# Kernel tuning notes

Hardware: AMD Instinct MI355X
Metric: run time of the kernel (lower is better)

The kernel has to match this reference:

```python
import jax, jax.numpy as jnp
import numpy as np

NUM_HEADS = 16
SIZE_PER_HEAD = 64
HIDDEN = NUM_HEADS * SIZE_PER_HEAD  # 1024
B, F, T = 4, 1024, 1024
NEG_INF = -10000.0


def setup_inputs() -> dict:
    key = jax.random.key(0)
    ks = jax.random.split(key, 6)
    scale = 0.02
    return {
        "from_tensor": jax.random.normal(ks[0], (B, F, HIDDEN), dtype=jnp.float32),
        "to_tensor": jax.random.normal(ks[1], (B, T, HIDDEN), dtype=jnp.float32),
        "attention_mask": jnp.ones((B, F, T), dtype=jnp.float32),
        "Wq": jax.random.normal(ks[2], (HIDDEN, HIDDEN), dtype=jnp.float32) * scale,
        "bq": jnp.zeros((HIDDEN,), dtype=jnp.float32),
        "Wk": jax.random.normal(ks[3], (HIDDEN, HIDDEN), dtype=jnp.float32) * scale,
        "bk": jnp.zeros((HIDDEN,), dtype=jnp.float32),
        "Wv": jax.random.normal(ks[4], (HIDDEN, HIDDEN), dtype=jnp.float32) * scale,
        "bv": jnp.zeros((HIDDEN,), dtype=jnp.float32),
    }


def _split_heads(x, seq_len):
    # [B, S, H*Dh] -> [B, H, S, Dh]
    return x.reshape(B, seq_len, NUM_HEADS, SIZE_PER_HEAD).transpose(0, 2, 1, 3)


def reference(from_tensor, to_tensor, attention_mask, Wq, bq, Wk, bk, Wv, bv):
    # Q/K/V dense projections (query_act/key_act/value_act are None -> linear)
    q = _split_heads(from_tensor @ Wq + bq, F)   # [B,H,F,Dh]
    k = _split_heads(to_tensor @ Wk + bk, T)     # [B,H,T,Dh]
    v = _split_heads(to_tensor @ Wv + bv, T)     # [B,H,T,Dh]

    # scaled dot-product attention scores: [B,H,F,T]
    scores = jnp.einsum("bhfd,bhtd->bhft", q, k) / jnp.sqrt(
        jnp.asarray(SIZE_PER_HEAD, dtype=q.dtype))

    # BERT-style mask adder: mask==1 -> attend, mask==0 -> -10000
    adder = (1.0 - attention_mask[:, None, :, :]) * NEG_INF
    scores = scores + adder

    attention_probs = jax.nn.softmax(scores, axis=-1)  # dropout_prob=0.0

    ctx = jnp.einsum("bhft,bhtd->bhfd", attention_probs, v)  # [B,H,F,Dh]
    ctx = ctx.transpose(0, 2, 1, 3).reshape(B, F, NUM_HEADS * SIZE_PER_HEAD)
    return ctx, attention_probs
```

## Files before the change

### kernel.cpp

```cpp
#include <hip/hip_runtime.h>

typedef unsigned short u16;
typedef __bf16 bf16x8 __attribute__((ext_vector_type(8)));
typedef float f32x4 __attribute__((ext_vector_type(4)));
typedef u16 u16x8 __attribute__((ext_vector_type(8)));
typedef u16 u16x4 __attribute__((ext_vector_type(4)));

#define NUM_HEADS 16
#define HIDDEN 1024
#define BATCH 4
#define SEQ 1024
#define C1 0.1803368809109783f
#define LOG2E 1.4426950408889634f

#define VMCNT0 asm volatile("s_waitcnt vmcnt(0)" ::: "memory")

static __device__ __forceinline__ u16 f2bf(float x) {
  unsigned u = __float_as_uint(x);
  u = u + 0x7FFFu + ((u >> 16) & 1u);
  return (u16)(u >> 16);
}
static __device__ __forceinline__ float bf2f(u16 b) {
  return __uint_as_float(((unsigned)b) << 16);
}
static __device__ __forceinline__ void async16(u16* lds, const u16* g) {
  __builtin_amdgcn_global_load_lds(
      (const __attribute__((address_space(1))) void*)g,
      (__attribute__((address_space(3))) void*)lds, 16, 0, 0);
}

__global__ void k_cvt(const float* __restrict__ in0, u16* __restrict__ out0,
                      const float* __restrict__ in1, u16* __restrict__ out1, int n8) {
  int i = blockIdx.x * 256 + threadIdx.x;
  if (i >= n8) return;
  const float* in = blockIdx.z ? in1 : in0;
  u16* out = blockIdx.z ? out1 : out0;
  float4 a = ((const float4*)in)[i * 2];
  float4 b = ((const float4*)in)[i * 2 + 1];
  u16x8 v;
  v[0] = f2bf(a.x); v[1] = f2bf(a.y); v[2] = f2bf(a.z); v[3] = f2bf(a.w);
  v[4] = f2bf(b.x); v[5] = f2bf(b.y); v[6] = f2bf(b.z); v[7] = f2bf(b.w);
  *(u16x8*)&out[(size_t)i * 8] = v;
}

__global__ void k_wtrans(const float* __restrict__ Wq, const float* __restrict__ Wk,
                         const float* __restrict__ Wv, u16* __restrict__ Wt) {
  __shared__ float tile[64][65];
  const float* W = (blockIdx.z == 0) ? Wq : (blockIdx.z == 1) ? Wk : Wv;
  u16* out = Wt + (size_t)blockIdx.z * HIDDEN * HIDDEN;
  int k0 = blockIdx.y * 64, n0 = blockIdx.x * 64;
  int tid = threadIdx.x;
  int r = tid >> 6, c = tid & 63;
#pragma unroll
  for (int i = 0; i < 16; ++i)
    tile[i * 4 + r][c] = W[(size_t)(k0 + i * 4 + r) * HIDDEN + n0 + c];
  __syncthreads();
#pragma unroll
  for (int i = 0; i < 16; ++i)
    out[(size_t)(n0 + i * 4 + r) * HIDDEN + k0 + c] = f2bf(tile[c][i * 4 + r]);
}

__global__ void k_mask(const float* __restrict__ mask, u16* __restrict__ adder,
                       int* __restrict__ flags) {
  int tt = blockIdx.x, ft = blockIdx.y, b = blockIdx.z;
  int tid = threadIdx.x;
  __shared__ int sflag;
  if (tid == 0) sflag = 0;
  __syncthreads();
  size_t base = ((size_t)b * SEQ + ft * 128) * SEQ + tt * 128;
  int any = 0;
#pragma unroll
  for (int i = 0; i < 16; ++i) {
    int idx = i * 256 + tid;
    int r = idx >> 5, c4 = idx & 31;
    float4 v = *(const float4*)&mask[base + (size_t)r * SEQ + c4 * 4];
    any |= (v.x != 1.0f) | (v.y != 1.0f) | (v.z != 1.0f) | (v.w != 1.0f);
  }
  if (any) sflag = 1;
  __syncthreads();
  if (sflag) {
#pragma unroll
    for (int i = 0; i < 16; ++i) {
      int idx = i * 256 + tid;
      int r = idx >> 5, c4 = idx & 31;
      float4 v = *(const float4*)&mask[base + (size_t)r * SEQ + c4 * 4];
      u16x4 o;
      o[0] = f2bf((1.0f - v.x) * -10000.0f * LOG2E);
      o[1] = f2bf((1.0f - v.y) * -10000.0f * LOG2E);
      o[2] = f2bf((1.0f - v.z) * -10000.0f * LOG2E);
      o[3] = f2bf((1.0f - v.w) * -10000.0f * LOG2E);
      *(u16x4*)&adder[base + (size_t)r * SEQ + c4 * 4] = o;
    }
  }
  if (tid == 0) flags[(b * 8 + ft) * 8 + tt] = sflag;
}

__global__ __launch_bounds__(256) void k_gemm(
    const u16* __restrict__ Af, const u16* __restrict__ At,
    const u16* __restrict__ Wt,
    const float* __restrict__ bq, const float* __restrict__ bk, const float* __restrict__ bv,
    u16* __restrict__ Qh, u16* __restrict__ Kh, u16* __restrict__ Vt) {
  __shared__ u16 sAB[2 * 128 * 64];
  u16* sA = sAB;
  u16* sB = sAB + 128 * 64;
  int which = blockIdx.z;
  const u16* A = (which == 0) ? Af : At;
  const u16* B = Wt + (size_t)which * HIDDEN * HIDDEN;
  const float* bias = (which == 0) ? bq : (which == 1) ? bk : bv;
  int wg = blockIdx.x + 8 * blockIdx.y;
  int xcd = wg & 7, j = wg >> 3;
  int ntile = j & 7, mstrip = xcd * 4 + (j >> 3);
  int m0 = mstrip * 128, n0 = ntile * 128;
  int tid = threadIdx.x, w = tid >> 6, lane = tid & 63;
  int wr = w >> 1, wc = w & 1;
  int g = lane >> 4, cc = lane & 15;

  f32x4 acc[4][4] = {};

  int sx[4], srow[4], scol[4];
#pragma unroll
  for (int i = 0; i < 4; ++i) {
    int ch = w * 4 + i;
    int x = ch * 1024 + lane * 16;
    int row = x >> 7;
    int colb = (x & 127) ^ ((row & 7) << 4);
    sx[i] = ch * 512;
    srow[i] = row;
    scol[i] = colb >> 1;
  }

  for (int kt = 0; kt < HIDDEN / 64; ++kt) {
    __syncthreads();
#pragma unroll
    for (int i = 0; i < 4; ++i) {
      async16(&sA[sx[i]], A + (size_t)(m0 + srow[i]) * HIDDEN + kt * 64 + scol[i]);
      async16(&sB[sx[i]], B + (size_t)(n0 + srow[i]) * HIDDEN + kt * 64 + scol[i]);
    }
    VMCNT0;
    __syncthreads();
#pragma unroll
    for (int kk = 0; kk < 2; ++kk) {
      bf16x8 af[4], bfr[4];
#pragma unroll
      for (int mf = 0; mf < 4; ++mf) {
        int row = wr * 64 + mf * 16 + cc;
        int colb = (kk * 64 + (g << 4)) ^ ((row & 7) << 4);
        af[mf] = *(const bf16x8*)&sA[(row * 128 + colb) >> 1];
      }
#pragma unroll
      for (int nf = 0; nf < 4; ++nf) {
        int row = wc * 64 + nf * 16 + cc;
        int colb = (kk * 64 + (g << 4)) ^ ((row & 7) << 4);
        bfr[nf] = *(const bf16x8*)&sB[(row * 128 + colb) >> 1];
      }
#pragma unroll
      for (int mf = 0; mf < 4; ++mf)
#pragma unroll
        for (int nf = 0; nf < 4; ++nf)
          acc[mf][nf] = __builtin_amdgcn_mfma_f32_16x16x32_bf16(af[mf], bfr[nf], acc[mf][nf], 0, 0, 0);
    }
  }

  if (which != 2) {
#pragma unroll
    for (int mf = 0; mf < 4; ++mf) {
#pragma unroll
      for (int nf = 0; nf < 4; ++nf) {
        int n = n0 + wc * 64 + nf * 16 + cc;
        float bval = bias[n];
        int h = n >> 6, d = n & 63;
#pragma unroll
        for (int r = 0; r < 4; ++r) {
          int m = m0 + wr * 64 + mf * 16 + g * 4 + r;
          int b = m >> 10, s = m & 1023;
          u16 o = f2bf(acc[mf][nf][r] + bval);
          if (which == 0)
            Qh[((((size_t)b * NUM_HEADS + h) * SEQ + s) << 6) + d] = o;
          else
            Kh[((((size_t)b * NUM_HEADS + h) * SEQ + s) << 6) + d] = o;
        }
      }
    }
  } else {
    __syncthreads();
    char* T = (char*)sAB;
#pragma unroll
    for (int mf = 0; mf < 4; ++mf) {
#pragma unroll
      for (int nf = 0; nf < 4; ++nf) {
        int nl = wc * 64 + nf * 16 + cc;
        float bval = bias[n0 + nl];
        int mlb = wr * 64 + mf * 16 + g * 4;
        u16x4 v;
#pragma unroll
        for (int r = 0; r < 4; ++r) v[r] = f2bf(acc[mf][nf][r] + bval);
        int byte = nl * 256 + ((mlb * 2) ^ ((nl & 7) << 4));
        *(u16x4*)(T + byte) = v;
      }
    }
    __syncthreads();
    int nl = tid >> 1, mh = (tid & 1) * 64;
    int b = m0 >> 10, s0 = m0 & 1023;
    u16* dst = &Vt[((size_t)b * 1024 + n0 + nl) * SEQ + s0 + mh];
#pragma unroll
    for (int j2 = 0; j2 < 8; ++j2) {
      int byte = nl * 256 + (((mh + j2 * 8) * 2) ^ ((nl & 7) << 4));
      *(u16x8*)&dst[j2 * 8] = *(const u16x8*)(T + byte);
    }
  }
}

__global__ __launch_bounds__(256) void k_attn(
    const u16* __restrict__ Qh, const u16* __restrict__ Kh, const u16* __restrict__ Vt,
    const u16* __restrict__ adder, const int* __restrict__ flags,
    float* __restrict__ ctx, float* __restrict__ probs) {
  __shared__ u16 sQ[128 * 64];
  __shared__ u16 sK[128 * 64];
  __shared__ u16 sV[64 * 128];
  __shared__ u16 sP[128 * 128];
  int wg = blockIdx.x;
  int logical = (wg & 7) * 64 + (wg >> 3);
  int ft = logical & 7, h = (logical >> 3) & 15, b = logical >> 7;
  int f0 = ft * 128;
  int bh = b * NUM_HEADS + h;
  const u16* Qg = Qh + ((size_t)bh * SEQ + f0) * 64;
  const u16* Kg = Kh + (size_t)bh * SEQ * 64;
  const u16* Vg = Vt + (size_t)bh * 64 * SEQ;
  int tid = threadIdx.x, w = tid >> 6, lane = tid & 63;
  int g = lane >> 4, cc = lane & 15;
  const int fbase = w * 32;

  int flgmask = 0;
#pragma unroll
  for (int tt = 0; tt < 8; ++tt)
    flgmask |= (flags[(b * 8 + ft) * 8 + tt] != 0) << tt;

  int sx[4], srow7[4], scol7[4], srow8[4], scol8[4];
#pragma unroll
  for (int i = 0; i < 4; ++i) {
    int ch = w * 4 + i;
    int x = ch * 1024 + lane * 16;
    sx[i] = ch * 512;
    int r7 = x >> 7;
    int c7 = (x & 127) ^ ((r7 & 7) << 4);
    srow7[i] = r7; scol7[i] = c7 >> 1;
    int r8 = x >> 8;
    int c8 = (x & 255) ^ ((r8 & 7) << 4);
    srow8[i] = r8; scol8[i] = c8 >> 1;
  }

#pragma unroll
  for (int i = 0; i < 4; ++i)
    async16(&sQ[sx[i]], Qg + (size_t)srow7[i] * 64 + scol7[i]);

  float l_run[8];
#pragma unroll
  for (int i = 0; i < 8; ++i) l_run[i] = 0.0f;

  for (int tt = 0; tt < 8; ++tt) {
    __syncthreads();
#pragma unroll
    for (int i = 0; i < 4; ++i)
      async16(&sK[sx[i]], Kg + (size_t)(tt * 128 + srow7[i]) * 64 + scol7[i]);
    VMCNT0;
    __syncthreads();

    f32x4 s[2][8] = {};
#pragma unroll
    for (int kk = 0; kk < 2; ++kk) {
      bf16x8 aq[2], bk8[8];
#pragma unroll
      for (int mf = 0; mf < 2; ++mf) {
        int row = fbase + mf * 16 + cc;
        int colb = (kk * 64 + (g << 4)) ^ ((row & 7) << 4);
        aq[mf] = *(const bf16x8*)&sQ[(row * 128 + colb) >> 1];
      }
#pragma unroll
      for (int nf = 0; nf < 8; ++nf) {
        int row = nf * 16 + cc;
        int colb = (kk * 64 + (g << 4)) ^ ((row & 7) << 4);
        bk8[nf] = *(const bf16x8*)&sK[(row * 128 + colb) >> 1];
      }
#pragma unroll
      for (int mf = 0; mf < 2; ++mf)
#pragma unroll
        for (int nf = 0; nf < 8; ++nf)
          s[mf][nf] = __builtin_amdgcn_mfma_f32_16x16x32_bf16(aq[mf], bk8[nf], s[mf][nf], 0, 0, 0);
    }
#pragma unroll
    for (int mf = 0; mf < 2; ++mf)
#pragma unroll
      for (int nf = 0; nf < 8; ++nf)
        s[mf][nf] = s[mf][nf] * C1;
    if ((flgmask >> tt) & 1) {
      for (int mf = 0; mf < 2; ++mf)
        for (int nf = 0; nf < 8; ++nf)
          for (int r = 0; r < 4; ++r) {
            int frow = f0 + fbase + mf * 16 + g * 4 + r;
            int tcol = tt * 128 + nf * 16 + cc;
            s[mf][nf][r] += bf2f(adder[((size_t)b * SEQ + frow) * SEQ + tcol]);
          }
    }
#pragma unroll
    for (int mf = 0; mf < 2; ++mf)
#pragma unroll
      for (int r = 0; r < 4; ++r) {
        float sum = 0.f;
#pragma unroll
        for (int nf = 0; nf < 8; ++nf) sum += exp2f(s[mf][nf][r]);
        sum += __shfl_xor(sum, 1, 16);
        sum += __shfl_xor(sum, 2, 16);
        sum += __shfl_xor(sum, 4, 16);
        sum += __shfl_xor(sum, 8, 16);
        l_run[mf * 4 + r] += sum;
      }
  }

  float inv_l[8];
#pragma unroll
  for (int i = 0; i < 8; ++i) inv_l[i] = 1.0f / l_run[i];

  f32x4 accO[2][4] = {};

  for (int tt = 0; tt < 8; ++tt) {
    __syncthreads();
#pragma unroll
    for (int i = 0; i < 4; ++i) {
      async16(&sK[sx[i]], Kg + (size_t)(tt * 128 + srow7[i]) * 64 + scol7[i]);
      async16(&sV[sx[i]], Vg + (size_t)srow8[i] * SEQ + tt * 128 + scol8[i]);
    }
    VMCNT0;
    __syncthreads();

    f32x4 s[2][8] = {};
#pragma unroll
    for (int kk = 0; kk < 2; ++kk) {
      bf16x8 aq[2], bk8[8];
#pragma unroll
      for (int mf = 0; mf < 2; ++mf) {
        int row = fbase + mf * 16 + cc;
        int colb = (kk * 64 + (g << 4)) ^ ((row & 7) << 4);
        aq[mf] = *(const bf16x8*)&sQ[(row * 128 + colb) >> 1];
      }
#pragma unroll
      for (int nf = 0; nf < 8; ++nf) {
        int row = nf * 16 + cc;
        int colb = (kk * 64 + (g << 4)) ^ ((row & 7) << 4);
        bk8[nf] = *(const bf16x8*)&sK[(row * 128 + colb) >> 1];
      }
#pragma unroll
      for (int mf = 0; mf < 2; ++mf)
#pragma unroll
        for (int nf = 0; nf < 8; ++nf)
          s[mf][nf] = __builtin_amdgcn_mfma_f32_16x16x32_bf16(aq[mf], bk8[nf], s[mf][nf], 0, 0, 0);
    }
#pragma unroll
    for (int mf = 0; mf < 2; ++mf)
#pragma unroll
      for (int nf = 0; nf < 8; ++nf)
        s[mf][nf] = s[mf][nf] * C1;
    if ((flgmask >> tt) & 1) {
      for (int mf = 0; mf < 2; ++mf)
        for (int nf = 0; nf < 8; ++nf)
          for (int r = 0; r < 4; ++r) {
            int frow = f0 + fbase + mf * 16 + g * 4 + r;
            int tcol = tt * 128 + nf * 16 + cc;
            s[mf][nf][r] += bf2f(adder[((size_t)b * SEQ + frow) * SEQ + tcol]);
          }
    }
#pragma unroll
    for (int mf = 0; mf < 2; ++mf)
#pragma unroll
      for (int nf = 0; nf < 8; ++nf)
#pragma unroll
        for (int r = 0; r < 4; ++r) {
          int idx = mf * 4 + r;
          float p = exp2f(s[mf][nf][r]) * inv_l[idx];
          int frow = fbase + mf * 16 + g * 4 + r;
          int tcol = nf * 16 + cc;
          probs[(((size_t)bh * SEQ) + f0 + frow) * SEQ + tt * 128 + tcol] = p;
          sP[(frow * 256 + ((tcol * 2) ^ ((frow & 7) << 4))) >> 1] = f2bf(p);
        }
#pragma unroll
    for (int ks = 0; ks < 4; ++ks) {
      bf16x8 ap[2], bv8[4];
#pragma unroll
      for (int mf = 0; mf < 2; ++mf) {
        int row = fbase + mf * 16 + cc;
        int colb = (ks * 64 + (g << 4)) ^ ((row & 7) << 4);
        ap[mf] = *(const bf16x8*)&sP[(row * 256 + colb) >> 1];
      }
#pragma unroll
      for (int nf = 0; nf < 4; ++nf) {
        int row = nf * 16 + cc;
        int colb = (ks * 64 + (g << 4)) ^ ((row & 7) << 4);
        bv8[nf] = *(const bf16x8*)&sV[(row * 256 + colb) >> 1];
      }
#pragma unroll
      for (int mf = 0; mf < 2; ++mf)
#pragma unroll
        for (int nf = 0; nf < 4; ++nf)
          accO[mf][nf] = __builtin_amdgcn_mfma_f32_16x16x32_bf16(ap[mf], bv8[nf], accO[mf][nf], 0, 0, 0);
    }
  }

#pragma unroll
  for (int mf = 0; mf < 2; ++mf)
#pragma unroll
    for (int nf = 0; nf < 4; ++nf)
#pragma unroll
      for (int r = 0; r < 4; ++r) {
        int frow = fbase + mf * 16 + g * 4 + r;
        int d = nf * 16 + cc;
        ctx[((size_t)b * SEQ + f0 + frow) * HIDDEN + h * 64 + d] = accO[mf][nf][r];
      }
}

extern "C" void kernel_launch(void* const* d_in, const int* in_sizes, int n_in,
                              void* d_out, int out_size, void* d_ws, size_t ws_size,
                              hipStream_t stream) {
  const float* from = (const float*)d_in[0];
  const float* to   = (const float*)d_in[1];
  const float* mask = (const float*)d_in[2];
  const float* Wq   = (const float*)d_in[3];
  const float* bq   = (const float*)d_in[4];
  const float* Wk   = (const float*)d_in[5];
  const float* bk   = (const float*)d_in[6];
  const float* Wv   = (const float*)d_in[7];
  const float* bv   = (const float*)d_in[8];

  char* ws = (char*)d_ws;
  u16* Af    = (u16*)(ws);
  u16* At    = (u16*)(ws + 8388608);
  u16* Wt    = (u16*)(ws + 16777216);
  u16* adder = (u16*)(ws + 23068672);
  int* flags = (int*)(ws + 31457280);
  u16* Qh    = (u16*)(ws + 31458304);
  u16* Kh    = (u16*)(ws + 39846912);
  u16* Vt    = (u16*)(ws + 48235520);

  float* ctx = (float*)d_out;
  float* probs = ctx + (size_t)BATCH * SEQ * HIDDEN;

  k_cvt<<<dim3(2048, 1, 2), 256, 0, stream>>>(from, Af, to, At, 524288);
  k_wtrans<<<dim3(16, 16, 3), 256, 0, stream>>>(Wq, Wk, Wv, Wt);
  k_mask<<<dim3(8, 8, 4), 256, 0, stream>>>(mask, adder, flags);
  k_gemm<<<dim3(8, 32, 3), 256, 0, stream>>>(Af, At, Wt, bq, bk, bv, Qh, Kh, Vt);
  k_attn<<<512, 256, 0, stream>>>(Qh, Kh, Vt, adder, flags, ctx, probs);
}
```

Baseline: 210.9 us.

## Merge prep kernels and split attention into row-sum and output passes

Fuses the three preprocessing kernels (input convert, weight transpose, mask adder) into one launch indexed by block id. The attention kernel is split in two: a lighter kernel with a 3-blocks-per-CU launch bound computes the softmax denominators and writes them to workspace, and the main kernel reads them instead of recomputing. The aim is to cut launch overhead and raise occupancy for the row-sum pass, at the cost of an extra launch and a global round trip for the inverse sums. The XCD-aware block remapping in the attention kernel is dropped in favour of a plain 3D grid.

```diff
diff --git a/kernel.cpp b/kernel.cpp
--- a/kernel.cpp
+++ b/kernel.cpp
@@ -29,70 +29,73 @@
       (__attribute__((address_space(3))) void*)lds, 16, 0, 0);
 }
 
-__global__ void k_cvt(const float* __restrict__ in0, u16* __restrict__ out0,
-                      const float* __restrict__ in1, u16* __restrict__ out1, int n8) {
-  int i = blockIdx.x * 256 + threadIdx.x;
-  if (i >= n8) return;
-  const float* in = blockIdx.z ? in1 : in0;
-  u16* out = blockIdx.z ? out1 : out0;
-  float4 a = ((const float4*)in)[i * 2];
-  float4 b = ((const float4*)in)[i * 2 + 1];
-  u16x8 v;
-  v[0] = f2bf(a.x); v[1] = f2bf(a.y); v[2] = f2bf(a.z); v[3] = f2bf(a.w);
-  v[4] = f2bf(b.x); v[5] = f2bf(b.y); v[6] = f2bf(b.z); v[7] = f2bf(b.w);
-  *(u16x8*)&out[(size_t)i * 8] = v;
-}
-
-__global__ void k_wtrans(const float* __restrict__ Wq, const float* __restrict__ Wk,
-                         const float* __restrict__ Wv, u16* __restrict__ Wt) {
-  __shared__ float tile[64][65];
-  const float* W = (blockIdx.z == 0) ? Wq : (blockIdx.z == 1) ? Wk : Wv;
-  u16* out = Wt + (size_t)blockIdx.z * HIDDEN * HIDDEN;
-  int k0 = blockIdx.y * 64, n0 = blockIdx.x * 64;
+__global__ __launch_bounds__(256) void k_prep(
+    const float* __restrict__ from, u16* __restrict__ Af,
+    const float* __restrict__ to, u16* __restrict__ At,
+    const float* __restrict__ Wq, const float* __restrict__ Wk,
+    const float* __restrict__ Wv, u16* __restrict__ Wt,
+    const float* __restrict__ mask, u16* __restrict__ adder, int* __restrict__ flags) {
+  int bid = blockIdx.x;
   int tid = threadIdx.x;
-  int r = tid >> 6, c = tid & 63;
-#pragma unroll
-  for (int i = 0; i < 16; ++i)
-    tile[i * 4 + r][c] = W[(size_t)(k0 + i * 4 + r) * HIDDEN + n0 + c];
-  __syncthreads();
-#pragma unroll
-  for (int i = 0; i < 16; ++i)
-    out[(size_t)(n0 + i * 4 + r) * HIDDEN + k0 + c] = f2bf(tile[c][i * 4 + r]);
-}
-
-__global__ void k_mask(const float* __restrict__ mask, u16* __restrict__ adder,
-                       int* __restrict__ flags) {
-  int tt = blockIdx.x, ft = blockIdx.y, b = blockIdx.z;
-  int tid = threadIdx.x;
-  __shared__ int sflag;
-  if (tid == 0) sflag = 0;
-  __syncthreads();
-  size_t base = ((size_t)b * SEQ + ft * 128) * SEQ + tt * 128;
-  int any = 0;
-#pragma unroll
-  for (int i = 0; i < 16; ++i) {
-    int idx = i * 256 + tid;
-    int r = idx >> 5, c4 = idx & 31;
-    float4 v = *(const float4*)&mask[base + (size_t)r * SEQ + c4 * 4];
-    any |= (v.x != 1.0f) | (v.y != 1.0f) | (v.z != 1.0f) | (v.w != 1.0f);
-  }
-  if (any) sflag = 1;
-  __syncthreads();
-  if (sflag) {
+  if (bid < 4096) {
+    const float* in = (bid < 2048) ? from : to;
+    u16* out = (bid < 2048) ? Af : At;
+    int i = (bid & 2047) * 256 + tid;
+    float4 a = ((const float4*)in)[i * 2];
+    float4 b = ((const float4*)in)[i * 2 + 1];
+    u16x8 v;
+    v[0] = f2bf(a.x); v[1] = f2bf(a.y); v[2] = f2bf(a.z); v[3] = f2bf(a.w);
+    v[4] = f2bf(b.x); v[5] = f2bf(b.y); v[6] = f2bf(b.z); v[7] = f2bf(b.w);
+    *(u16x8*)&out[(size_t)i * 8] = v;
+  } else if (bid < 4864) {
+    __shared__ float tile[64][65];
+    int wid = bid - 4096;
+    int z = wid >> 8, rem = wid & 255;
+    int x = rem & 15, y = rem >> 4;
+    const float* W = (z == 0) ? Wq : (z == 1) ? Wk : Wv;
+    u16* out = Wt + (size_t)z * HIDDEN * HIDDEN;
+    int k0 = y * 64, n0 = x * 64;
+    int r = tid >> 6, c = tid & 63;
+#pragma unroll
+    for (int i = 0; i < 16; ++i)
+      tile[i * 4 + r][c] = W[(size_t)(k0 + i * 4 + r) * HIDDEN + n0 + c];
+    __syncthreads();
+#pragma unroll
+    for (int i = 0; i < 16; ++i)
+      out[(size_t)(n0 + i * 4 + r) * HIDDEN + k0 + c] = f2bf(tile[c][i * 4 + r]);
+  } else {
+    int wid = bid - 4864;
+    int tt = wid & 7, ft = (wid >> 3) & 7, b = wid >> 6;
+    __shared__ int sflag;
+    if (tid == 0) sflag = 0;
+    __syncthreads();
+    size_t base = ((size_t)b * SEQ + ft * 128) * SEQ + tt * 128;
+    int any = 0;
 #pragma unroll
     for (int i = 0; i < 16; ++i) {
       int idx = i * 256 + tid;
       int r = idx >> 5, c4 = idx & 31;
       float4 v = *(const float4*)&mask[base + (size_t)r * SEQ + c4 * 4];
-      u16x4 o;
-      o[0] = f2bf((1.0f - v.x) * -10000.0f * LOG2E);
-      o[1] = f2bf((1.0f - v.y) * -10000.0f * LOG2E);
-      o[2] = f2bf((1.0f - v.z) * -10000.0f * LOG2E);
-      o[3] = f2bf((1.0f - v.w) * -10000.0f * LOG2E);
-      *(u16x4*)&adder[base + (size_t)r * SEQ + c4 * 4] = o;
-    }
-  }
-  if (tid == 0) flags[(b * 8 + ft) * 8 + tt] = sflag;
+      any |= (v.x != 1.0f) | (v.y != 1.0f) | (v.z != 1.0f) | (v.w != 1.0f);
+    }
+    if (any) sflag = 1;
+    __syncthreads();
+    if (sflag) {
+#pragma unroll
+      for (int i = 0; i < 16; ++i) {
+        int idx = i * 256 + tid;
+        int r = idx >> 5, c4 = idx & 31;
+        float4 v = *(const float4*)&mask[base + (size_t)r * SEQ + c4 * 4];
+        u16x4 o;
+        o[0] = f2bf((1.0f - v.x) * -10000.0f * LOG2E);
+        o[1] = f2bf((1.0f - v.y) * -10000.0f * LOG2E);
+        o[2] = f2bf((1.0f - v.z) * -10000.0f * LOG2E);
+        o[3] = f2bf((1.0f - v.w) * -10000.0f * LOG2E);
+        *(u16x4*)&adder[base + (size_t)r * SEQ + c4 * 4] = o;
+      }
+    }
+    if (tid == 0) flags[(b * 8 + ft) * 8 + tt] = sflag;
+  }
 }
 
 __global__ __launch_bounds__(256) void k_gemm(
@@ -210,17 +213,124 @@
   }
 }
 
-__global__ __launch_bounds__(256) void k_attn(
+__global__ __launch_bounds__(256, 3) void k_attn1(
+    const u16* __restrict__ Qh, const u16* __restrict__ Kh,
+    const u16* __restrict__ adder, const int* __restrict__ flags,
+    float* __restrict__ invl) {
+  __shared__ u16 sQ[128 * 64];
+  __shared__ u16 sK[128 * 64];
+  int ft = blockIdx.x, h = blockIdx.y, b = blockIdx.z;
+  int f0 = ft * 128;
+  int bh = b * NUM_HEADS + h;
+  const u16* Qg = Qh + ((size_t)bh * SEQ + f0) * 64;
+  const u16* Kg = Kh + (size_t)bh * SEQ * 64;
+  int tid = threadIdx.x, w = tid >> 6, lane = tid & 63;
+  int g = lane >> 4, cc = lane & 15;
+  const int fbase = w * 32;
+
+  int flgmask = 0;
+#pragma unroll
+  for (int tt = 0; tt < 8; ++tt)
+    flgmask |= (flags[(b * 8 + ft) * 8 + tt] != 0) << tt;
+
+  int sx[4], srow7[4], scol7[4];
+#pragma unroll
+  for (int i = 0; i < 4; ++i) {
+    int ch = w * 4 + i;
+    int x = ch * 1024 + lane * 16;
+    sx[i] = ch * 512;
+    int r7 = x >> 7;
+    int c7 = (x & 127) ^ ((r7 & 7) << 4);
+    srow7[i] = r7; scol7[i] = c7 >> 1;
+  }
+
+#pragma unroll
+  for (int i = 0; i < 4; ++i)
+    async16(&sQ[sx[i]], Qg + (size_t)srow7[i] * 64 + scol7[i]);
+
+  float l_run[8];
+#pragma unroll
+  for (int i = 0; i < 8; ++i) l_run[i] = 0.0f;
+
+  for (int tt = 0; tt < 8; ++tt) {
+    __syncthreads();
+#pragma unroll
+    for (int i = 0; i < 4; ++i)
+      async16(&sK[sx[i]], Kg + (size_t)(tt * 128 + srow7[i]) * 64 + scol7[i]);
+    VMCNT0;
+    __syncthreads();
+
+    f32x4 s[2][8] = {};
+#pragma unroll
+    for (int kk = 0; kk < 2; ++kk) {
+      bf16x8 aq[2], bk8[8];
+#pragma unroll
+      for (int mf = 0; mf < 2; ++mf) {
+        int row = fbase + mf * 16 + cc;
+        int colb = (kk * 64 + (g << 4)) ^ ((row & 7) << 4);
+        aq[mf] = *(const bf16x8*)&sQ[(row * 128 + colb) >> 1];
+      }
+#pragma unroll
+      for (int nf = 0; nf < 8; ++nf) {
+        int row = nf * 16 + cc;
+        int colb = (kk * 64 + (g << 4)) ^ ((row & 7) << 4);
+        bk8[nf] = *(const bf16x8*)&sK[(row * 128 + colb) >> 1];
+      }
+#pragma unroll
+      for (int mf = 0; mf < 2; ++mf)
+#pragma unroll
+        for (int nf = 0; nf < 8; ++nf)
+          s[mf][nf] = __builtin_amdgcn_mfma_f32_16x16x32_bf16(aq[mf], bk8[nf], s[mf][nf], 0, 0, 0);
+    }
+#pragma unroll
+    for (int mf = 0; mf < 2; ++mf)
+#pragma unroll
+      for (int nf = 0; nf < 8; ++nf)
+        s[mf][nf] = s[mf][nf] * C1;
+    if ((flgmask >> tt) & 1) {
+      for (int mf = 0; mf < 2; ++mf)
+        for (int nf = 0; nf < 8; ++nf)
+          for (int r = 0; r < 4; ++r) {
+            int frow = f0 + fbase + mf * 16 + g * 4 + r;
+            int tcol = tt * 128 + nf * 16 + cc;
+            s[mf][nf][r] += bf2f(adder[((size_t)b * SEQ + frow) * SEQ + tcol]);
+          }
+    }
+#pragma unroll
+    for (int mf = 0; mf < 2; ++mf)
+#pragma unroll
+      for (int r = 0; r < 4; ++r) {
+        float sum = 0.f;
+#pragma unroll
+        for (int nf = 0; nf < 8; ++nf) sum += exp2f(s[mf][nf][r]);
+        sum += __shfl_xor(sum, 1, 16);
+        sum += __shfl_xor(sum, 2, 16);
+        sum += __shfl_xor(sum, 4, 16);
+        sum += __shfl_xor(sum, 8, 16);
+        l_run[mf * 4 + r] += sum;
+      }
+  }
+
+  if (cc == 0) {
+#pragma unroll
+    for (int mf = 0; mf < 2; ++mf)
+#pragma unroll
+      for (int r = 0; r < 4; ++r)
+        invl[(size_t)bh * SEQ + f0 + fbase + mf * 16 + g * 4 + r] =
+            1.0f / l_run[mf * 4 + r];
+  }
+}
+
+__global__ __launch_bounds__(256) void k_attn2(
     const u16* __restrict__ Qh, const u16* __restrict__ Kh, const u16* __restrict__ Vt,
     const u16* __restrict__ adder, const int* __restrict__ flags,
+    const float* __restrict__ invl,
     float* __restrict__ ctx, float* __restrict__ probs) {
   __shared__ u16 sQ[128 * 64];
   __shared__ u16 sK[128 * 64];
   __shared__ u16 sV[64 * 128];
   __shared__ u16 sP[128 * 128];
-  int wg = blockIdx.x;
-  int logical = (wg & 7) * 64 + (wg >> 3);
-  int ft = logical & 7, h = (logical >> 3) & 15, b = logical >> 7;
+  int ft = blockIdx.x, h = blockIdx.y, b = blockIdx.z;
   int f0 = ft * 128;
   int bh = b * NUM_HEADS + h;
   const u16* Qg = Qh + ((size_t)bh * SEQ + f0) * 64;
@@ -253,72 +363,13 @@
   for (int i = 0; i < 4; ++i)
     async16(&sQ[sx[i]], Qg + (size_t)srow7[i] * 64 + scol7[i]);
 
-  float l_run[8];
-#pragma unroll
-  for (int i = 0; i < 8; ++i) l_run[i] = 0.0f;
-
-  for (int tt = 0; tt < 8; ++tt) {
-    __syncthreads();
-#pragma unroll
-    for (int i = 0; i < 4; ++i)
-      async16(&sK[sx[i]], Kg + (size_t)(tt * 128 + srow7[i]) * 64 + scol7[i]);
-    VMCNT0;
-    __syncthreads();
-
-    f32x4 s[2][8] = {};
-#pragma unroll
-    for (int kk = 0; kk < 2; ++kk) {
-      bf16x8 aq[2], bk8[8];
-#pragma unroll
-      for (int mf = 0; mf < 2; ++mf) {
-        int row = fbase + mf * 16 + cc;
-        int colb = (kk * 64 + (g << 4)) ^ ((row & 7) << 4);
-        aq[mf] = *(const bf16x8*)&sQ[(row * 128 + colb) >> 1];
-      }
-#pragma unroll
-      for (int nf = 0; nf < 8; ++nf) {
-        int row = nf * 16 + cc;
-        int colb = (kk * 64 + (g << 4)) ^ ((row & 7) << 4);
-        bk8[nf] = *(const bf16x8*)&sK[(row * 128 + colb) >> 1];
-      }
-#pragma unroll
-      for (int mf = 0; mf < 2; ++mf)
-#pragma unroll
-        for (int nf = 0; nf < 8; ++nf)
-          s[mf][nf] = __builtin_amdgcn_mfma_f32_16x16x32_bf16(aq[mf], bk8[nf], s[mf][nf], 0, 0, 0);
-    }
-#pragma unroll
-    for (int mf = 0; mf < 2; ++mf)
-#pragma unroll
-      for (int nf = 0; nf < 8; ++nf)
-        s[mf][nf] = s[mf][nf] * C1;
-    if ((flgmask >> tt) & 1) {
-      for (int mf = 0; mf < 2; ++mf)
-        for (int nf = 0; nf < 8; ++nf)
-          for (int r = 0; r < 4; ++r) {
-            int frow = f0 + fbase + mf * 16 + g * 4 + r;
-            int tcol = tt * 128 + nf * 16 + cc;
-            s[mf][nf][r] += bf2f(adder[((size_t)b * SEQ + frow) * SEQ + tcol]);
-          }
-    }
-#pragma unroll
-    for (int mf = 0; mf < 2; ++mf)
-#pragma unroll
-      for (int r = 0; r < 4; ++r) {
-        float sum = 0.f;
-#pragma unroll
-        for (int nf = 0; nf < 8; ++nf) sum += exp2f(s[mf][nf][r]);
-        sum += __shfl_xor(sum, 1, 16);
-        sum += __shfl_xor(sum, 2, 16);
-        sum += __shfl_xor(sum, 4, 16);
-        sum += __shfl_xor(sum, 8, 16);
-        l_run[mf * 4 + r] += sum;
-      }
-  }
-
   float inv_l[8];
 #pragma unroll
-  for (int i = 0; i < 8; ++i) inv_l[i] = 1.0f / l_run[i];
+  for (int mf = 0; mf < 2; ++mf)
+#pragma unroll
+    for (int r = 0; r < 4; ++r)
+      inv_l[mf * 4 + r] =
+          invl[(size_t)bh * SEQ + f0 + fbase + mf * 16 + g * 4 + r];
 
   f32x4 accO[2][4] = {};
 
@@ -438,13 +489,13 @@
   u16* Qh    = (u16*)(ws + 31458304);
   u16* Kh    = (u16*)(ws + 39846912);
   u16* Vt    = (u16*)(ws + 48235520);
+  float* invl = (float*)(ws);
 
   float* ctx = (float*)d_out;
   float* probs = ctx + (size_t)BATCH * SEQ * HIDDEN;
 
-  k_cvt<<<dim3(2048, 1, 2), 256, 0, stream>>>(from, Af, to, At, 524288);
-  k_wtrans<<<dim3(16, 16, 3), 256, 0, stream>>>(Wq, Wk, Wv, Wt);
-  k_mask<<<dim3(8, 8, 4), 256, 0, stream>>>(mask, adder, flags);
+  k_prep<<<5120, 256, 0, stream>>>(from, Af, to, At, Wq, Wk, Wv, Wt, mask, adder, flags);
   k_gemm<<<dim3(8, 32, 3), 256, 0, stream>>>(Af, At, Wt, bq, bk, bv, Qh, Kh, Vt);
-  k_attn<<<512, 256, 0, stream>>>(Qh, Kh, Vt, adder, flags, ctx, probs);
-}
+  k_attn1<<<dim3(8, 16, 4), 256, 0, stream>>>(Qh, Kh, adder, flags, invl);
+  k_attn2<<<dim3(8, 16, 4), 256, 0, stream>>>(Qh, Kh, Vt, adder, flags, invl, ctx, probs);
+}
```

Result: faster. 205.0 us (-2.8%).
